# Performance work log

Measured on AMD Instinct MI355X. Metric: run time of the kernel, lower is better.

Reference implementation:

```python
import jax, jax.numpy as jnp
import numpy as np

E, D, H = 1024, 64, 16   # embed_dim, head_dim, num_heads
B, L = 8, 4096


def _ln(x, g, b, eps=1e-5):
    m = jnp.mean(x, axis=-1, keepdims=True)
    v = jnp.var(x, axis=-1, keepdims=True)
    return (x - m) / jnp.sqrt(v + eps) * g + b


def setup_inputs() -> dict:
    key = jax.random.key(0)
    ks = jax.random.split(key, 10)
    s_e = 1.0 / np.sqrt(E)
    s_d = 1.0 / np.sqrt(D)
    f32 = jnp.float32
    return {
        "emb": jax.random.normal(ks[0], (B, L, E), f32),
        # per-head linears stacked on a leading head axis
        "Wa": jax.random.normal(ks[1], (H, E, D), f32) * s_e,
        "ba": jnp.zeros((H, D), f32),
        "Wb": jax.random.normal(ks[2], (H, E, D), f32) * s_e,
        "bb": jnp.zeros((H, D), f32),
        "Wc": jax.random.normal(ks[3], (H, D, D), f32) * s_d,
        "bc": jnp.zeros((H, D), f32),
        "head_w": jnp.ones((H,), f32),
        "hn_g": jnp.ones((H, D), f32),
        "hn_b": jnp.zeros((H, D), f32),
        "Wd": jax.random.normal(ks[4], (E, D), f32) * s_e,
        "bd": jnp.zeros((D,), f32),
        "W1": jax.random.normal(ks[5], (D, 4 * D), f32) * s_d,
        "b1": jnp.zeros((4 * D,), f32),
        "W2": jax.random.normal(ks[6], (4 * D, D), f32) * (1.0 / np.sqrt(4 * D)),
        "b2": jnp.zeros((D,), f32),
        "Wp": jax.random.normal(ks[7], (D, D), f32) * s_d,
        "bp": jnp.zeros((D,), f32),
        "ng": jnp.ones((D,), f32),
        "nb": jnp.zeros((D,), f32),
    }


def reference(emb, Wa, ba, Wb, bb, Wc, bc, head_w, hn_g, hn_b,
              Wd, bd, W1, b1, W2, b2, Wp, bp, ng, nb):
    b_sz, seq_len, _ = emb.shape
    n_heads, d_head = ba.shape

    # gates depend only on x_t -> precompute for all t, all heads  [B,L,H,D]
    a = jnp.tanh(jnp.einsum('ble,hed->blhd', emb, Wa) + ba)
    bt = jnp.einsum('ble,hed->blhd', emb, Wb) + bb

    # linear recurrence h_t = a_t * h_{t-1} + b_t over time
    a_t = jnp.moveaxis(a, 1, 0)    # [L,B,H,D]
    b_t = jnp.moveaxis(bt, 1, 0)

    def step(h, ab):
        at, btt = ab
        h = at * h + btt
        return h, h

    h0 = jnp.zeros((b_sz, n_heads, d_head), emb.dtype)
    _, hs = jax.lax.scan(step, h0, (a_t, b_t))
    hs = jnp.moveaxis(hs, 0, 1)    # [B,L,H,D]

    dx = emb @ Wd + bd             # [B,L,D] shared D(x_t)

    out = jnp.einsum('blhd,hde->blhe', hs, Wc) + bc + dx[:, :, None, :]
    out = _ln(out, hn_g, hn_b)     # per-head LayerNorm, gamma/beta [H,D]

    sum_heads = dx + jnp.einsum('h,blhd->bld', head_w, out)
    z = sum_heads / n_heads

    u = z + _ln(z, ng, nb)
    ffn = jax.nn.gelu(u @ W1 + b1, approximate=False) @ W2 + b2
    h_out = u + ffn
    return h_out @ Wp + bp
```

## Files before the change

kernel.cpp:

```cpp
#include <hip/hip_runtime.h>
#include <hip/hip_bf16.h>
#include <math.h>
#include <stdint.h>

#define E_DIM 1024
#define D_DIM 64
#define H_DIM 16
#define B_SZ  8
#define L_SEQ 4096
#define M_TOK (B_SZ * L_SEQ)
#define NCAT  2112
#define NPAD  2176
#define CHUNK 128
#define NCHUNK (L_SEQ / CHUNK)

typedef float  f32x4  __attribute__((ext_vector_type(4)));
typedef __bf16 bf16x8 __attribute__((ext_vector_type(8)));
typedef __bf16 bf16x4 __attribute__((ext_vector_type(4)));

__device__ __forceinline__ float tanh_fast(float v) {
  float vc = fminf(fmaxf(v, -12.f), 12.f);
  float ex = __expf(vc + vc);
  return (ex - 1.f) / (ex + 1.f);
}
__device__ __forceinline__ void load_lds16(const void* g, void* l) {
  __builtin_amdgcn_global_load_lds(
      (const __attribute__((address_space(1))) void*)g,
      (__attribute__((address_space(3))) void*)l, 16, 0, 0);
}

__global__ __launch_bounds__(256) void cast_emb(const float* __restrict__ in,
                                                bf16x4* __restrict__ out) {
  int i = blockIdx.x * 256 + threadIdx.x;
  float4 v = ((const float4*)in)[i];
  bf16x4 o;
  o[0] = (__bf16)v.x; o[1] = (__bf16)v.y; o[2] = (__bf16)v.z; o[3] = (__bf16)v.w;
  out[i] = o;
}

__global__ __launch_bounds__(256) void pack_w(
    const float* __restrict__ Wa, const float* __restrict__ ba,
    const float* __restrict__ Wb, const float* __restrict__ bb,
    const float* __restrict__ Wd, const float* __restrict__ bd,
    __bf16* __restrict__ wcat, float* __restrict__ bias) {
  int gid = blockIdx.x * 256 + threadIdx.x;
  int n = gid >> 10, k = gid & 1023;
  float w, bv;
  if (n < 1024) {
    int h = n >> 6, d = n & 63;
    w = Wa[((h << 10) | k) * 64 + d]; bv = ba[n];
  } else if (n < 2048) {
    int nn = n - 1024; int h = nn >> 6, d = nn & 63;
    w = Wb[((h << 10) | k) * 64 + d]; bv = bb[nn];
  } else if (n < NCAT) {
    int d = n - 2048;
    w = Wd[k * 64 + d];  bv = bd[d];
  } else { w = 0.f; bv = 0.f; }
  wcat[n * 1024 + k] = (__bf16)w;
  if (k == 0) bias[n] = bv;
}

__global__ __launch_bounds__(256) void pack_ffnw(
    const float* __restrict__ W1, const float* __restrict__ W2,
    const float* __restrict__ Wp,
    __bf16* __restrict__ g_w1t, __bf16* __restrict__ g_w2t,
    __bf16* __restrict__ g_wpt) {
  int idx = blockIdx.x * 256 + threadIdx.x;
  if (idx < 16384) {
    int k = idx >> 8, n = idx & 255;
    g_w1t[n * 72 + k] = (__bf16)W1[idx];
  } else if (idx < 32768) {
    int j = idx - 16384; int k = j >> 6, n = j & 63;
    g_w2t[n * 256 + (((k >> 3) ^ (n & 7)) << 3) + (k & 7)] = (__bf16)W2[j];
  } else {
    int j = idx - 32768; int k = j >> 6, n = j & 63;
    g_wpt[n * 72 + k] = (__bf16)Wp[j];
  }
}

__global__ __launch_bounds__(256) void pack_wct(const float* __restrict__ Wc,
                                                __bf16* __restrict__ wct) {
  int idx = blockIdx.x * 256 + threadIdx.x;
  int h = idx >> 12, e = (idx >> 6) & 63, d = idx & 63;
  wct[idx] = (__bf16)Wc[h * 4096 + d * 64 + e];
}

__global__ __launch_bounds__(256) void gemm_fused(
    const __bf16* __restrict__ A, const __bf16* __restrict__ Wt,
    const float* __restrict__ bias,
    __bf16* __restrict__ abuf, __bf16* __restrict__ bbuf, float* __restrict__ dxbuf) {
  __shared__ __bf16 As[128 * 64];
  __shared__ __bf16 Bs[128 * 64];
  const int nt = blockIdx.x, mt = blockIdx.y;
  const int m0 = mt * 128, n0 = nt * 128;
  const int t = threadIdx.x, w = t >> 6, l = t & 63;
  const int lr = l >> 3, lc = l & 7;
  const int swz = lc ^ lr;
  const int q = l >> 4, c16 = l & 15;

  f32x4 acc[4][4];
#pragma unroll
  for (int i = 0; i < 4; ++i)
#pragma unroll
    for (int j = 0; j < 4; ++j) acc[i][j] = (f32x4)(0.f);

  const __bf16* gA = A  + (size_t)(m0 + w * 8 + lr) * 1024 + swz * 8;
  const __bf16* gB = Wt + (size_t)(n0 + w * 8 + lr) * 1024 + swz * 8;
  __bf16* lA = As + w * 512;
  __bf16* lB = Bs + w * 512;

  for (int kk = 0; kk < 16; ++kk) {
    const int k0 = kk * 64;
#pragma unroll
    for (int r = 0; r < 4; ++r) {
      load_lds16(gA + (size_t)r * 32 * 1024 + k0, lA + r * 2048);
      load_lds16(gB + (size_t)r * 32 * 1024 + k0, lB + r * 2048);
    }
    __syncthreads();
#pragma unroll
    for (int ks = 0; ks < 2; ++ks) {
      bf16x8 af[4], bfr[4];
#pragma unroll
      for (int i = 0; i < 4; ++i) {
        int mloc = (w >> 1) * 64 + i * 16 + c16;
        int cp = (ks * 4 + q) ^ (mloc & 7);
        af[i] = *(const bf16x8*)(As + mloc * 64 + cp * 8);
      }
#pragma unroll
      for (int j = 0; j < 4; ++j) {
        int nloc = (w & 1) * 64 + j * 16 + c16;
        int cp = (ks * 4 + q) ^ (nloc & 7);
        bfr[j] = *(const bf16x8*)(Bs + nloc * 64 + cp * 8);
      }
#pragma unroll
      for (int i = 0; i < 4; ++i)
#pragma unroll
        for (int j = 0; j < 4; ++j)
          acc[i][j] = __builtin_amdgcn_mfma_f32_16x16x32_bf16(af[i], bfr[j], acc[i][j], 0, 0, 0);
    }
    __syncthreads();
  }

#pragma unroll
  for (int j = 0; j < 4; ++j) {
    int n = n0 + (w & 1) * 64 + j * 16 + c16;
    float bv = bias[n];
#pragma unroll
    for (int i = 0; i < 4; ++i) {
      int mbase = m0 + (w >> 1) * 64 + i * 16 + q * 4;
#pragma unroll
      for (int r = 0; r < 4; ++r) {
        float v = acc[i][j][r] + bv;
        int m = mbase + r;
        if (n < 1024)            abuf[(size_t)m * 1024 + n] = (__bf16)tanh_fast(v);
        else if (n < 2048)       bbuf[(size_t)m * 1024 + (n - 1024)] = (__bf16)v;
        else if (n < NCAT)       dxbuf[m * 64 + (n - 2048)] = v;
      }
    }
  }
}

__global__ __launch_bounds__(256) void scan_local_bf(
    __bf16* __restrict__ abuf, __bf16* __restrict__ bbuf,
    float* __restrict__ cA, float* __restrict__ cH) {
  int bc = blockIdx.x;
  int n4 = threadIdx.x * 4;
  size_t base = (size_t)bc * CHUNK * 1024 + n4;
  float p[4] = {1.f, 1.f, 1.f, 1.f}, h[4] = {0.f, 0.f, 0.f, 0.f};
  for (int s = 0; s < CHUNK; ++s) {
    size_t idx = base + (size_t)s * 1024;
    bf16x4 av = *(const bf16x4*)(abuf + idx);
    bf16x4 bv = *(const bf16x4*)(bbuf + idx);
    bf16x4 po, ho;
#pragma unroll
    for (int i = 0; i < 4; ++i) {
      float a = (float)av[i];
      p[i] *= a;
      h[i] = fmaf(a, h[i], (float)bv[i]);
      po[i] = (__bf16)p[i];
      ho[i] = (__bf16)h[i];
    }
    *(bf16x4*)(abuf + idx) = po;
    *(bf16x4*)(bbuf + idx) = ho;
  }
  int ci = bc * 1024 + n4;
  float4 pv = {p[0], p[1], p[2], p[3]};
  float4 hv = {h[0], h[1], h[2], h[3]};
  *(float4*)(cA + ci) = pv;
  *(float4*)(cH + ci) = hv;
}

__global__ __launch_bounds__(256) void scan_carry(
    const float* __restrict__ cA, const float* __restrict__ cH, float* __restrict__ cIn) {
  int gid = blockIdx.x * 256 + threadIdx.x;
  int n = gid & 1023, b = gid >> 10;
  float carry = 0.f;
  for (int c = 0; c < NCHUNK; ++c) {
    int idx = (b * NCHUNK + c) * 1024 + n;
    cIn[idx] = carry;
    carry = fmaf(cA[idx], carry, cH[idx]);
  }
}

__global__ __launch_bounds__(256) void heads_mfma(
    const __bf16* __restrict__ ahat, const __bf16* __restrict__ hloc,
    const float* __restrict__ dxbuf, const float* __restrict__ cIn,
    const __bf16* __restrict__ wct, const float* __restrict__ bch,
    const float* __restrict__ head_w, const float* __restrict__ hng,
    const float* __restrict__ hnb, const float* __restrict__ ng,
    const float* __restrict__ nbv, float* __restrict__ ubuf) {
  __shared__ float carryS[1024];
  const int tid = threadIdx.x, w = tid >> 6, l = tid & 63;
  const int q = l >> 4, c16 = l & 15;
  const int m0 = blockIdx.x * 64;
  const int b = m0 >> 12, c = (m0 & 4095) >> 7;
  const int cb = (b * NCHUNK + c) * 1024;
  ((float4*)carryS)[tid] = ((const float4*)(cIn + cb))[tid];
  __syncthreads();

  const size_t arow = (size_t)(m0 + w * 16 + c16) * 1024;

  float dxr[4][4];
#pragma unroll
  for (int j = 0; j < 4; ++j)
#pragma unroll
    for (int r = 0; r < 4; ++r)
      dxr[j][r] = dxbuf[(m0 + w * 16 + q * 4 + r) * 64 + j * 16 + c16];

  f32x4 accum[4];
#pragma unroll
  for (int j = 0; j < 4; ++j) accum[j] = (f32x4)(0.f);

  for (int h = 0; h < H_DIM; ++h) {
    bf16x8 af[2];
#pragma unroll
    for (int ks = 0; ks < 2; ++ks) {
      int dbase = h * 64 + ks * 32 + q * 8;
      bf16x8 av = *(const bf16x8*)(ahat + arow + dbase);
      bf16x8 hv = *(const bf16x8*)(hloc + arow + dbase);
      float4 cv0 = *(const float4*)(carryS + dbase);
      float4 cv1 = *(const float4*)(carryS + dbase + 4);
      bf16x8 hf;
      hf[0] = (__bf16)fmaf((float)av[0], cv0.x, (float)hv[0]);
      hf[1] = (__bf16)fmaf((float)av[1], cv0.y, (float)hv[1]);
      hf[2] = (__bf16)fmaf((float)av[2], cv0.z, (float)hv[2]);
      hf[3] = (__bf16)fmaf((float)av[3], cv0.w, (float)hv[3]);
      hf[4] = (__bf16)fmaf((float)av[4], cv1.x, (float)hv[4]);
      hf[5] = (__bf16)fmaf((float)av[5], cv1.y, (float)hv[5]);
      hf[6] = (__bf16)fmaf((float)av[6], cv1.z, (float)hv[6]);
      hf[7] = (__bf16)fmaf((float)av[7], cv1.w, (float)hv[7]);
      af[ks] = hf;
    }
    f32x4 acc[4];
#pragma unroll
    for (int j = 0; j < 4; ++j) acc[j] = (f32x4)(0.f);
#pragma unroll
    for (int ks = 0; ks < 2; ++ks)
#pragma unroll
      for (int j = 0; j < 4; ++j) {
        bf16x8 bf = *(const bf16x8*)(wct + h * 4096 + (j * 16 + c16) * 64 + ks * 32 + q * 8);
        acc[j] = __builtin_amdgcn_mfma_f32_16x16x32_bf16(af[ks], bf, acc[j], 0, 0, 0);
      }
    float hw = head_w[h];
    float g4[4], be4[4], bb4[4];
#pragma unroll
    for (int j = 0; j < 4; ++j) {
      int nh = h * 64 + j * 16 + c16;
      g4[j] = hng[nh]; bb4[j] = hnb[nh]; be4[j] = bch[nh];
    }
#pragma unroll
    for (int r = 0; r < 4; ++r) {
      float v0 = acc[0][r] + be4[0] + dxr[0][r];
      float v1 = acc[1][r] + be4[1] + dxr[1][r];
      float v2 = acc[2][r] + be4[2] + dxr[2][r];
      float v3 = acc[3][r] + be4[3] + dxr[3][r];
      float s  = (v0 + v1) + (v2 + v3);
      float s2 = fmaf(v0, v0, fmaf(v1, v1, fmaf(v2, v2, v3 * v3)));
#pragma unroll
      for (int off = 1; off < 16; off <<= 1) {
        s  += __shfl_xor(s, off, 64);
        s2 += __shfl_xor(s2, off, 64);
      }
      float mean = s * (1.f / 64.f);
      float var  = fmaf(s2, 1.f / 64.f, -mean * mean);
      float inv  = rsqrtf(fmaxf(var, 0.f) + 1e-5f);
      accum[0][r] = fmaf(hw, fmaf((v0 - mean) * inv, g4[0], bb4[0]), accum[0][r]);
      accum[1][r] = fmaf(hw, fmaf((v1 - mean) * inv, g4[1], bb4[1]), accum[1][r]);
      accum[2][r] = fmaf(hw, fmaf((v2 - mean) * inv, g4[2], bb4[2]), accum[2][r]);
      accum[3][r] = fmaf(hw, fmaf((v3 - mean) * inv, g4[3], bb4[3]), accum[3][r]);
    }
  }
  float ng4[4], nb4[4];
#pragma unroll
  for (int j = 0; j < 4; ++j) { ng4[j] = ng[j * 16 + c16]; nb4[j] = nbv[j * 16 + c16]; }
#pragma unroll
  for (int r = 0; r < 4; ++r) {
    float z0 = (dxr[0][r] + accum[0][r]) * (1.f / 16.f);
    float z1 = (dxr[1][r] + accum[1][r]) * (1.f / 16.f);
    float z2 = (dxr[2][r] + accum[2][r]) * (1.f / 16.f);
    float z3 = (dxr[3][r] + accum[3][r]) * (1.f / 16.f);
    float s  = (z0 + z1) + (z2 + z3);
    float s2 = fmaf(z0, z0, fmaf(z1, z1, fmaf(z2, z2, z3 * z3)));
#pragma unroll
    for (int off = 1; off < 16; off <<= 1) {
      s  += __shfl_xor(s, off, 64);
      s2 += __shfl_xor(s2, off, 64);
    }
    float mean = s * (1.f / 64.f);
    float var  = fmaf(s2, 1.f / 64.f, -mean * mean);
    float inv  = rsqrtf(fmaxf(var, 0.f) + 1e-5f);
    int mrow = (m0 + w * 16 + q * 4 + r) * 64;
    ubuf[mrow + 0 * 16 + c16] = z0 + fmaf((z0 - mean) * inv, ng4[0], nb4[0]);
    ubuf[mrow + 1 * 16 + c16] = z1 + fmaf((z1 - mean) * inv, ng4[1], nb4[1]);
    ubuf[mrow + 2 * 16 + c16] = z2 + fmaf((z2 - mean) * inv, ng4[2], nb4[2]);
    ubuf[mrow + 3 * 16 + c16] = z3 + fmaf((z3 - mean) * inv, ng4[3], nb4[3]);
  }
}

__global__ __launch_bounds__(256) void ffn_mfma(
    const float* __restrict__ ubuf,
    const __bf16* __restrict__ g_w1t, const __bf16* __restrict__ g_w2t,
    const __bf16* __restrict__ g_wpt,
    const float* __restrict__ b1, const float* __restrict__ b2,
    const float* __restrict__ bp, float* __restrict__ out) {
  __shared__ __bf16 pool[32768];
  const int tid = threadIdx.x, w = tid >> 6, l = tid & 63;
  const int q = l >> 4, c16 = l & 15;
  const int m0 = blockIdx.x * 64;
  __bf16* Us  = pool;
  __bf16* W1T = pool + 4608;
  __bf16* T1S = pool;
  __bf16* W2T = pool + 16384;
  __bf16* HoS = pool;
  __bf16* WpT = pool + 4608;

#pragma unroll
  for (int r = 0; r < 16; ++r) {
    int idx = r * 256 + tid, m = idx >> 6, e = idx & 63;
    Us[m * 72 + e] = (__bf16)ubuf[(size_t)(m0 + m) * 64 + e];
  }
#pragma unroll
  for (int r = 0; r < 9; ++r)
    load_lds16(g_w1t + (size_t)(r * 256 + tid) * 8,
               (char*)pool + 9216 + (r * 256 + w * 64) * 16);
  __syncthreads();

  f32x4 acc1[16];
#pragma unroll
  for (int j = 0; j < 16; ++j) acc1[j] = (f32x4)(0.f);
#pragma unroll
  for (int ks = 0; ks < 2; ++ks) {
    bf16x8 a = *(const bf16x8*)(Us + (w * 16 + c16) * 72 + ks * 32 + q * 8);
#pragma unroll
    for (int j = 0; j < 16; ++j) {
      bf16x8 b = *(const bf16x8*)(W1T + (j * 16 + c16) * 72 + ks * 32 + q * 8);
      acc1[j] = __builtin_amdgcn_mfma_f32_16x16x32_bf16(a, b, acc1[j], 0, 0, 0);
    }
  }
  __syncthreads();

#pragma unroll
  for (int r = 0; r < 8; ++r)
    load_lds16(g_w2t + (size_t)(r * 256 + tid) * 8,
               (char*)pool + 32768 + (r * 256 + w * 64) * 16);
#pragma unroll
  for (int j = 0; j < 16; ++j) {
    int n = j * 16 + c16;
    float bv = b1[n];
#pragma unroll
    for (int rr = 0; rr < 4; ++rr) {
      int m = w * 16 + q * 4 + rr;
      float x = acc1[j][rr] + bv;
      float g = 0.5f * x * (1.f + erff(x * 0.70710678118654752f));
      T1S[m * 256 + (((n >> 3) ^ (m & 7)) << 3) + (n & 7)] = (__bf16)g;
    }
  }
  __syncthreads();

  f32x4 acc2[4];
#pragma unroll
  for (int j = 0; j < 4; ++j) acc2[j] = (f32x4)(0.f);
  const int arow2 = w * 16 + c16;
#pragma unroll
  for (int ks = 0; ks < 8; ++ks) {
    bf16x8 a = *(const bf16x8*)(T1S + arow2 * 256 + (((ks * 4 + q) ^ (arow2 & 7)) << 3));
#pragma unroll
    for (int j = 0; j < 4; ++j) {
      int brow = j * 16 + c16;
      bf16x8 b = *(const bf16x8*)(W2T + brow * 256 + (((ks * 4 + q) ^ (brow & 7)) << 3));
      acc2[j] = __builtin_amdgcn_mfma_f32_16x16x32_bf16(a, b, acc2[j], 0, 0, 0);
    }
  }
  __syncthreads();

#pragma unroll
  for (int r = 0; r < 2; ++r)
    load_lds16(g_wpt + (size_t)(r * 256 + tid) * 8,
               (char*)pool + 9216 + (r * 256 + w * 64) * 16);
  if (tid < 64)
    load_lds16(g_wpt + (size_t)(512 + tid) * 8, (char*)pool + 9216 + 512 * 16);
#pragma unroll
  for (int j = 0; j < 4; ++j) {
    int e = j * 16 + c16;
    float bv = b2[e];
#pragma unroll
    for (int rr = 0; rr < 4; ++rr) {
      int m = w * 16 + q * 4 + rr;
      float hres = acc2[j][rr] + bv + ubuf[(size_t)(m0 + m) * 64 + e];
      HoS[m * 72 + e] = (__bf16)hres;
    }
  }
  __syncthreads();

  f32x4 acc3[4];
#pragma unroll
  for (int j = 0; j < 4; ++j) acc3[j] = (f32x4)(0.f);
#pragma unroll
  for (int ks = 0; ks < 2; ++ks) {
    bf16x8 a = *(const bf16x8*)(HoS + (w * 16 + c16) * 72 + ks * 32 + q * 8);
#pragma unroll
    for (int j = 0; j < 4; ++j) {
      bf16x8 b = *(const bf16x8*)(WpT + (j * 16 + c16) * 72 + ks * 32 + q * 8);
      acc3[j] = __builtin_amdgcn_mfma_f32_16x16x32_bf16(a, b, acc3[j], 0, 0, 0);
    }
  }
#pragma unroll
  for (int j = 0; j < 4; ++j) {
    int e = j * 16 + c16;
    float bv = bp[e];
#pragma unroll
    for (int rr = 0; rr < 4; ++rr) {
      int m = w * 16 + q * 4 + rr;
      out[(size_t)(m0 + m) * 64 + e] = acc3[j][rr] + bv;
    }
  }
}

extern "C" void kernel_launch(void* const* d_in, const int* in_sizes, int n_in,
                              void* d_out, int out_size, void* d_ws, size_t ws_size,
                              hipStream_t stream) {
  const float* emb    = (const float*)d_in[0];
  const float* Wa     = (const float*)d_in[1];
  const float* ba     = (const float*)d_in[2];
  const float* Wb     = (const float*)d_in[3];
  const float* bb     = (const float*)d_in[4];
  const float* Wc     = (const float*)d_in[5];
  const float* bc     = (const float*)d_in[6];
  const float* head_w = (const float*)d_in[7];
  const float* hn_g   = (const float*)d_in[8];
  const float* hn_b   = (const float*)d_in[9];
  const float* Wd     = (const float*)d_in[10];
  const float* bd     = (const float*)d_in[11];
  const float* W1     = (const float*)d_in[12];
  const float* b1     = (const float*)d_in[13];
  const float* W2     = (const float*)d_in[14];
  const float* b2     = (const float*)d_in[15];
  const float* Wp     = (const float*)d_in[16];
  const float* bp     = (const float*)d_in[17];
  const float* ng     = (const float*)d_in[18];
  const float* nb     = (const float*)d_in[19];
  float* out = (float*)d_out;

  char* wsp = (char*)d_ws;
  size_t off = 0;
  auto alloc = [&](size_t bytes) -> char* {
    char* p = wsp + off;
    off += (bytes + 255) & ~(size_t)255;
    return p;
  };
  __bf16* embh  = (__bf16*)alloc((size_t)M_TOK * E_DIM * 2);
  __bf16* wcat  = (__bf16*)alloc((size_t)NPAD * E_DIM * 2);
  float*  bias  = (float*)alloc((size_t)NPAD * 4);
  __bf16* abuf  = (__bf16*)alloc((size_t)M_TOK * 1024 * 2);
  __bf16* bbuf  = (__bf16*)alloc((size_t)M_TOK * 1024 * 2);
  float*  dxbuf = (float*)alloc((size_t)M_TOK * 64 * 4);
  float*  cA    = (float*)alloc((size_t)256 * 1024 * 4);
  float*  cH    = (float*)alloc((size_t)256 * 1024 * 4);
  float*  cIn   = (float*)alloc((size_t)256 * 1024 * 4);
  float*  ubuf  = (float*)alloc((size_t)M_TOK * 64 * 4);
  __bf16* g_w1t = (__bf16*)alloc((size_t)256 * 72 * 2);
  __bf16* g_w2t = (__bf16*)alloc((size_t)64 * 256 * 2);
  __bf16* g_wpt = (__bf16*)alloc((size_t)64 * 72 * 2);
  __bf16* wct   = (__bf16*)alloc((size_t)H_DIM * 64 * 64 * 2);

  cast_emb<<<dim3(32768), dim3(256), 0, stream>>>(emb, (bf16x4*)embh);
  pack_w<<<dim3(8704), dim3(256), 0, stream>>>(Wa, ba, Wb, bb, Wd, bd, wcat, bias);
  pack_ffnw<<<dim3(144), dim3(256), 0, stream>>>(W1, W2, Wp, g_w1t, g_w2t, g_wpt);
  pack_wct<<<dim3(256), dim3(256), 0, stream>>>(Wc, wct);
  gemm_fused<<<dim3(17, 256), dim3(256), 0, stream>>>(embh, wcat, bias, abuf, bbuf, dxbuf);
  scan_local_bf<<<dim3(256), dim3(256), 0, stream>>>(abuf, bbuf, cA, cH);
  scan_carry<<<dim3(32), dim3(256), 0, stream>>>(cA, cH, cIn);
  heads_mfma<<<dim3(512), dim3(256), 0, stream>>>(abuf, bbuf, dxbuf, cIn, wct, bc,
                                                  head_w, hn_g, hn_b, ng, nb, ubuf);
  ffn_mfma<<<dim3(512), dim3(256), 0, stream>>>(ubuf, g_w1t, g_w2t, g_wpt,
                                                b1, b2, bp, out);
}
```

Baseline: 602.4 us.

## Rewrite fused gate GEMM with 256x256 tiles and multi-stage LDS pipeline

Rewrites the main gate/bias/D GEMM to use 256x256 output tiles on 512-thread blocks, with a 4-slot LDS ring, async global-to-LDS prefetch several K-steps ahead, explicit vmcnt waits and barriers, s_setprio around the MFMA bursts, and an XCD-aware block remap. The aim is to hide global load latency and raise MFMA utilization in the dominant GEMM, at the cost of padding N to 2304, which adds wasted columns. The scan chunk size is also halved so the local scan launches more blocks, which means more carry entries to handle. The handwritten waitcnt accounting is fragile.

```diff
diff --git a/kernel.cpp b/kernel.cpp
--- a/kernel.cpp
+++ b/kernel.cpp
@@ -10,8 +10,8 @@
 #define L_SEQ 4096
 #define M_TOK (B_SZ * L_SEQ)
 #define NCAT  2112
-#define NPAD  2176
-#define CHUNK 128
+#define NPAD  2304
+#define CHUNK 64
 #define NCHUNK (L_SEQ / CHUNK)
 
 typedef float  f32x4  __attribute__((ext_vector_type(4)));
@@ -85,76 +85,108 @@
   wct[idx] = (__bf16)Wc[h * 4096 + d * 64 + e];
 }
 
-__global__ __launch_bounds__(256) void gemm_fused(
+__global__ __launch_bounds__(512, 2) void gemm_fused(
     const __bf16* __restrict__ A, const __bf16* __restrict__ Wt,
     const float* __restrict__ bias,
     __bf16* __restrict__ abuf, __bf16* __restrict__ bbuf, float* __restrict__ dxbuf) {
-  __shared__ __bf16 As[128 * 64];
-  __shared__ __bf16 Bs[128 * 64];
-  const int nt = blockIdx.x, mt = blockIdx.y;
-  const int m0 = mt * 128, n0 = nt * 128;
-  const int t = threadIdx.x, w = t >> 6, l = t & 63;
-  const int lr = l >> 3, lc = l & 7;
-  const int swz = lc ^ lr;
+  __shared__ __bf16 lds[65536];
+  const int id = blockIdx.x;
+  const int wg = (id & 7) * 144 + (id >> 3);
+  const int mt = wg / 9, nt = wg % 9;
+  const int m0 = mt * 256, n0 = nt * 256;
+  const int t = threadIdx.x;
+  const int w = t >> 6, l = t & 63;
+  const int wr = w >> 2, wc = w & 3;
   const int q = l >> 4, c16 = l & 15;
-
-  f32x4 acc[4][4];
-#pragma unroll
-  for (int i = 0; i < 4; ++i)
+  const int cp = q ^ ((c16 >> 1) & 3);
+  const int srow = l >> 2;
+  const int schk = (l & 3) ^ ((l >> 3) & 3);
+
+  f32x4 acc[8][4];
+#pragma unroll
+  for (int i = 0; i < 8; ++i)
 #pragma unroll
     for (int j = 0; j < 4; ++j) acc[i][j] = (f32x4)(0.f);
 
-  const __bf16* gA = A  + (size_t)(m0 + w * 8 + lr) * 1024 + swz * 8;
-  const __bf16* gB = Wt + (size_t)(n0 + w * 8 + lr) * 1024 + swz * 8;
-  __bf16* lA = As + w * 512;
-  __bf16* lB = Bs + w * 512;
-
-  for (int kk = 0; kk < 16; ++kk) {
-    const int k0 = kk * 64;
-#pragma unroll
-    for (int r = 0; r < 4; ++r) {
-      load_lds16(gA + (size_t)r * 32 * 1024 + k0, lA + r * 2048);
-      load_lds16(gB + (size_t)r * 32 * 1024 + k0, lB + r * 2048);
-    }
-    __syncthreads();
-#pragma unroll
-    for (int ks = 0; ks < 2; ++ks) {
-      bf16x8 af[4], bfr[4];
-#pragma unroll
-      for (int i = 0; i < 4; ++i) {
-        int mloc = (w >> 1) * 64 + i * 16 + c16;
-        int cp = (ks * 4 + q) ^ (mloc & 7);
-        af[i] = *(const bf16x8*)(As + mloc * 64 + cp * 8);
-      }
-#pragma unroll
-      for (int j = 0; j < 4; ++j) {
-        int nloc = (w & 1) * 64 + j * 16 + c16;
-        int cp = (ks * 4 + q) ^ (nloc & 7);
-        bfr[j] = *(const bf16x8*)(Bs + nloc * 64 + cp * 8);
-      }
-#pragma unroll
-      for (int i = 0; i < 4; ++i)
-#pragma unroll
-        for (int j = 0; j < 4; ++j)
-          acc[i][j] = __builtin_amdgcn_mfma_f32_16x16x32_bf16(af[i], bfr[j], acc[i][j], 0, 0, 0);
-    }
-    __syncthreads();
-  }
+  auto stage = [&](int H) {
+    int th = H >> 1, isB = H & 1, slot = th & 3;
+    const __bf16* src = isB ? Wt : A;
+    int base0 = isB ? n0 : m0;
+    int ldsbase = (isB ? 32768 : 0) + slot * 8192;
+#pragma unroll
+    for (int r = 0; r < 2; ++r) {
+      int rw = r * 128 + w * 16;
+      load_lds16(src + (size_t)(base0 + rw + srow) * 1024 + th * 32 + schk * 8,
+                 &lds[ldsbase + rw * 32]);
+    }
+  };
+
+  auto tile_phases = [&](int tt, bool sA, bool sB) {
+    const int slot = tt & 3;
+    const __bf16* Asl = lds + slot * 8192;
+    const __bf16* Bsl = lds + 32768 + slot * 8192;
+    bf16x8 bfr[4], af[4];
+#pragma unroll
+    for (int j = 0; j < 4; ++j)
+      bfr[j] = *(const bf16x8*)(Bsl + (wc * 64 + j * 16 + c16) * 32 + cp * 8);
+#pragma unroll
+    for (int i = 0; i < 4; ++i)
+      af[i] = *(const bf16x8*)(Asl + (wr * 128 + i * 16 + c16) * 32 + cp * 8);
+    if (sA) stage(2 * tt + 5);
+    __builtin_amdgcn_s_setprio(1);
+#pragma unroll
+    for (int i = 0; i < 4; ++i)
+#pragma unroll
+      for (int j = 0; j < 4; ++j)
+        acc[i][j] = __builtin_amdgcn_mfma_f32_16x16x32_bf16(af[i], bfr[j], acc[i][j], 0, 0, 0);
+    __builtin_amdgcn_s_setprio(0);
+    asm volatile("s_barrier" ::: "memory");
+#pragma unroll
+    for (int i = 0; i < 4; ++i)
+      af[i] = *(const bf16x8*)(Asl + (wr * 128 + (4 + i) * 16 + c16) * 32 + cp * 8);
+    if (sB) stage(2 * tt + 6);
+    __builtin_amdgcn_s_setprio(1);
+#pragma unroll
+    for (int i = 0; i < 4; ++i)
+#pragma unroll
+      for (int j = 0; j < 4; ++j)
+        acc[4 + i][j] = __builtin_amdgcn_mfma_f32_16x16x32_bf16(af[i], bfr[j], acc[4 + i][j], 0, 0, 0);
+    __builtin_amdgcn_s_setprio(0);
+  };
+
+  stage(0); stage(1); stage(2); stage(3); stage(4);
+  asm volatile("s_waitcnt vmcnt(6)" ::: "memory");
+  asm volatile("s_barrier" ::: "memory");
+
+#pragma unroll 1
+  for (int tt = 0; tt < 29; ++tt) {
+    tile_phases(tt, true, true);
+    asm volatile("s_waitcnt vmcnt(6)" ::: "memory");
+    asm volatile("s_barrier" ::: "memory");
+  }
+  tile_phases(29, true, false);
+  asm volatile("s_waitcnt vmcnt(4)" ::: "memory");
+  asm volatile("s_barrier" ::: "memory");
+  tile_phases(30, false, false);
+  asm volatile("s_waitcnt vmcnt(0)" ::: "memory");
+  asm volatile("s_barrier" ::: "memory");
+  tile_phases(31, false, false);
 
 #pragma unroll
   for (int j = 0; j < 4; ++j) {
-    int n = n0 + (w & 1) * 64 + j * 16 + c16;
+    int n = n0 + wc * 64 + j * 16 + c16;
+    if (n >= NCAT) continue;
     float bv = bias[n];
 #pragma unroll
-    for (int i = 0; i < 4; ++i) {
-      int mbase = m0 + (w >> 1) * 64 + i * 16 + q * 4;
+    for (int i = 0; i < 8; ++i) {
+      int mbase = m0 + wr * 128 + i * 16 + q * 4;
 #pragma unroll
       for (int r = 0; r < 4; ++r) {
         float v = acc[i][j][r] + bv;
         int m = mbase + r;
         if (n < 1024)            abuf[(size_t)m * 1024 + n] = (__bf16)tanh_fast(v);
         else if (n < 2048)       bbuf[(size_t)m * 1024 + (n - 1024)] = (__bf16)v;
-        else if (n < NCAT)       dxbuf[m * 64 + (n - 2048)] = v;
+        else                     dxbuf[m * 64 + (n - 2048)] = v;
       }
     }
   }
@@ -167,6 +199,7 @@
   int n4 = threadIdx.x * 4;
   size_t base = (size_t)bc * CHUNK * 1024 + n4;
   float p[4] = {1.f, 1.f, 1.f, 1.f}, h[4] = {0.f, 0.f, 0.f, 0.f};
+#pragma unroll 4
   for (int s = 0; s < CHUNK; ++s) {
     size_t idx = base + (size_t)s * 1024;
     bf16x4 av = *(const bf16x4*)(abuf + idx);
@@ -213,7 +246,7 @@
   const int tid = threadIdx.x, w = tid >> 6, l = tid & 63;
   const int q = l >> 4, c16 = l & 15;
   const int m0 = blockIdx.x * 64;
-  const int b = m0 >> 12, c = (m0 & 4095) >> 7;
+  const int b = m0 >> 12, c = (m0 & 4095) >> 6;
   const int cb = (b * NCHUNK + c) * 1024;
   ((float4*)carryS)[tid] = ((const float4*)(cIn + cb))[tid];
   __syncthreads();
@@ -474,9 +507,9 @@
   __bf16* abuf  = (__bf16*)alloc((size_t)M_TOK * 1024 * 2);
   __bf16* bbuf  = (__bf16*)alloc((size_t)M_TOK * 1024 * 2);
   float*  dxbuf = (float*)alloc((size_t)M_TOK * 64 * 4);
-  float*  cA    = (float*)alloc((size_t)256 * 1024 * 4);
-  float*  cH    = (float*)alloc((size_t)256 * 1024 * 4);
-  float*  cIn   = (float*)alloc((size_t)256 * 1024 * 4);
+  float*  cA    = (float*)alloc((size_t)512 * 1024 * 4);
+  float*  cH    = (float*)alloc((size_t)512 * 1024 * 4);
+  float*  cIn   = (float*)alloc((size_t)512 * 1024 * 4);
   float*  ubuf  = (float*)alloc((size_t)M_TOK * 64 * 4);
   __bf16* g_w1t = (__bf16*)alloc((size_t)256 * 72 * 2);
   __bf16* g_w2t = (__bf16*)alloc((size_t)64 * 256 * 2);
@@ -484,11 +517,11 @@
   __bf16* wct   = (__bf16*)alloc((size_t)H_DIM * 64 * 64 * 2);
 
   cast_emb<<<dim3(32768), dim3(256), 0, stream>>>(emb, (bf16x4*)embh);
-  pack_w<<<dim3(8704), dim3(256), 0, stream>>>(Wa, ba, Wb, bb, Wd, bd, wcat, bias);
+  pack_w<<<dim3(9216), dim3(256), 0, stream>>>(Wa, ba, Wb, bb, Wd, bd, wcat, bias);
   pack_ffnw<<<dim3(144), dim3(256), 0, stream>>>(W1, W2, Wp, g_w1t, g_w2t, g_wpt);
   pack_wct<<<dim3(256), dim3(256), 0, stream>>>(Wc, wct);
-  gemm_fused<<<dim3(17, 256), dim3(256), 0, stream>>>(embh, wcat, bias, abuf, bbuf, dxbuf);
-  scan_local_bf<<<dim3(256), dim3(256), 0, stream>>>(abuf, bbuf, cA, cH);
+  gemm_fused<<<dim3(1152), dim3(512), 0, stream>>>(embh, wcat, bias, abuf, bbuf, dxbuf);
+  scan_local_bf<<<dim3(512), dim3(256), 0, stream>>>(abuf, bbuf, cA, cH);
   scan_carry<<<dim3(32), dim3(256), 0, stream>>>(cA, cH, cIn);
   heads_mfma<<<dim3(512), dim3(256), 0, stream>>>(abuf, bbuf, dxbuf, cIn, wct, bc,
                                                   head_w, hn_g, hn_b, ng, nb, ubuf);
```

Result: no change. 600.5 us (-0.3%).
